# Kernel tuning notes

Measured on AMD Instinct MI355X. Metric: run time of the kernel, lower is better.

## Reference

```python
import jax, jax.numpy as jnp
import numpy as np

EMBED_DIM = 1024
B, T = 4, 2048

def setup_inputs() -> dict:
    key = jax.random.key(0)
    ks = jax.random.split(key, 7)
    s = 1.0 / np.sqrt(EMBED_DIM)
    return {
        "x": jax.random.normal(ks[0], (B, T, EMBED_DIM), dtype=jnp.float32),
        "Wq": jax.random.uniform(ks[1], (EMBED_DIM, EMBED_DIM), jnp.float32, -s, s),
        "bq": jax.random.uniform(ks[2], (EMBED_DIM,), jnp.float32, -s, s),
        "Wk": jax.random.uniform(ks[3], (EMBED_DIM, EMBED_DIM), jnp.float32, -s, s),
        "bk": jax.random.uniform(ks[4], (EMBED_DIM,), jnp.float32, -s, s),
        "Wv": jax.random.uniform(ks[5], (EMBED_DIM, EMBED_DIM), jnp.float32, -s, s),
        "bv": jax.random.uniform(ks[6], (EMBED_DIM,), jnp.float32, -s, s),
    }

def reference(x, Wq, bq, Wk, bk, Wv, bv):
    Bsz, Tlen, C = x.shape
    # torch Linear: y = x @ W.T + b
    Q = jnp.einsum('btc,dc->btd', x, Wq) + bq
    K = jnp.einsum('btc,dc->btd', x, Wk) + bk
    V = jnp.einsum('btc,dc->btd', x, Wv) + bv
    score = jnp.einsum('bqd,bkd->bqk', Q, K) / jnp.sqrt(jnp.float32(C))
    causal = jnp.tril(jnp.ones((Tlen, Tlen), dtype=bool))  # [T,T]
    score = jnp.where(causal, score, -jnp.inf)
    att = jax.nn.softmax(score, axis=-1)
    return jnp.einsum('bqk,bkd->bqd', att, V)
```

## Files before the change

kernel.cpp:

```cpp
#include <hip/hip_runtime.h>


using u16 = unsigned short;
typedef __attribute__((ext_vector_type(8))) short short8;
typedef __attribute__((ext_vector_type(4))) float f32x4;

__device__ __forceinline__ u16 f2b(float f) {
  unsigned u = __builtin_bit_cast(unsigned, f);
  u += 0x7fffu + ((u >> 16) & 1u);
  return (u16)(u >> 16);
}

__device__ __forceinline__ float b2f(u16 h) {
  return __builtin_bit_cast(float, (unsigned)h << 16);
}

__device__ __forceinline__ void async16(void* lds, const void* g) {
  __builtin_amdgcn_global_load_lds(
      (const __attribute__((address_space(1))) unsigned int*)g,
      (__attribute__((address_space(3))) unsigned int*)lds, 16, 0, 0);
}

__device__ __forceinline__ void block_barrier() {
  asm volatile("" ::: "memory");
  __builtin_amdgcn_s_barrier();
  asm volatile("" ::: "memory");
}

__global__ __launch_bounds__(256) void cvt_all_kernel(
    const float* __restrict__ x, const float* __restrict__ Wq,
    const float* __restrict__ Wk, const float* __restrict__ Wv,
    u16* __restrict__ xb, u16* __restrict__ Wcat) {
  const int i = blockIdx.x * 256 + threadIdx.x;
  const float* src;
  u16* dst;
  int c;
  if (i < 2097152) {
    src = x; dst = xb; c = i;
  } else {
    const int r = i - 2097152;
    const int seg = r >> 18;
    src = seg == 0 ? Wq : (seg == 1 ? Wk : Wv);
    dst = Wcat + (size_t)seg * 1048576;
    c = r & 262143;
  }
  const float4 v = reinterpret_cast<const float4*>(src)[c];
  ushort4 o;
  o.x = f2b(v.x); o.y = f2b(v.y); o.z = f2b(v.z); o.w = f2b(v.w);
  reinterpret_cast<ushort4*>(dst)[c] = o;
}

#define STG_A(buf, half, roff, ku)                                          \
  {                                                                         \
    async16(&Asm[buf][half][tid * 8], gA0 + (size_t)(roff)*lda + (ku));     \
    async16(&Asm[buf][half][4096 + tid * 8],                                \
            gA0 + (size_t)((roff) + 128) * lda + (ku));                     \
  }
#define STG_B(buf, half, roff, ku)                                          \
  {                                                                         \
    async16(&Bsm[buf][half][tid * 8], gB0 + (size_t)(roff)*ldb + (ku));     \
    async16(&Bsm[buf][half][4096 + tid * 8],                                \
            gB0 + (size_t)((roff) + 128) * ldb + (ku));                     \
  }
#define RD_A(buf, hh)                                                       \
  {                                                                         \
    _Pragma("unroll") for (int ii = 0; ii < 4; ++ii) {                      \
      a[ii][0] = *(const short8*)(&Asm[buf][hh][aoff + ii * 1024 + sk0]);   \
      a[ii][1] = *(const short8*)(&Asm[buf][hh][aoff + ii * 1024 + sk1]);   \
    }                                                                       \
  }
#define RD_B(buf, cc, breg)                                                 \
  {                                                                         \
    _Pragma("unroll") for (int jj = 0; jj < 2; ++jj) {                      \
      breg[jj][0] = *(const short8*)(&Bsm[buf][cc][boff + jj * 1024 + sk0]);\
      breg[jj][1] = *(const short8*)(&Bsm[buf][cc][boff + jj * 1024 + sk1]);\
    }                                                                       \
  }
#define QUAD(hh, cc, breg)                                                  \
  {                                                                         \
    __builtin_amdgcn_s_setprio(1);                                          \
    _Pragma("unroll") for (int ii = 0; ii < 4; ++ii)                        \
        _Pragma("unroll") for (int jj = 0; jj < 2; ++jj) {                  \
      acc[(hh)*4 + ii][(cc)*2 + jj] =                                       \
          __builtin_amdgcn_mfma_f32_16x16x32_bf16(                          \
              a[ii][0], breg[jj][0], acc[(hh)*4 + ii][(cc)*2 + jj], 0,0,0); \
      acc[(hh)*4 + ii][(cc)*2 + jj] =                                       \
          __builtin_amdgcn_mfma_f32_16x16x32_bf16(                          \
              a[ii][1], breg[jj][1], acc[(hh)*4 + ii][(cc)*2 + jj], 0,0,0); \
    }                                                                       \
    __builtin_amdgcn_s_setprio(0);                                          \
  }
#define LGK0 asm volatile("s_waitcnt lgkmcnt(0)" ::: "memory")
#define VM6 asm volatile("s_waitcnt vmcnt(6)" ::: "memory")

template <int NT, typename Epi>
__device__ __forceinline__ void gemm256_8ph(const u16* __restrict__ A, int lda,
                                            const u16* __restrict__ B, int ldb,
                                            Epi&& epi) {
  __shared__ __align__(16) u16 Asm[2][2][8192];
  __shared__ __align__(16) u16 Bsm[2][2][8192];
  const int tid = threadIdx.x;
  const int lane = tid & 63;
  const int w = tid >> 6;
  const int wm = w >> 2;
  const int wn = w & 3;

  f32x4 acc[8][4];
#pragma unroll
  for (int i = 0; i < 8; ++i)
#pragma unroll
    for (int j = 0; j < 4; ++j) acc[i][j] = f32x4{0.f, 0.f, 0.f, 0.f};

  const int sr = tid >> 3;
  const int ce = ((tid & 7) ^ (sr & 7)) << 3;
  const u16* gA0 = A + (size_t)sr * lda + ce;
  const int bE = (sr & 31) + ((sr >> 5) << 6);
  const u16* gB0 = B + (size_t)bE * ldb + ce;

  const int l15 = lane & 15;
  const int hi = lane >> 4;
  const int lo7 = lane & 7;
  const int aoff = wm * 4096 + l15 * 64;
  const int boff = wn * 2048 + l15 * 64;
  const int sk0 = (hi ^ lo7) << 3;
  const int sk1 = ((4 + hi) ^ lo7) << 3;

  short8 a[4][2], bEr[2][2], bLr[2][2];

  STG_A(0, 0, 0, 0); STG_B(0, 0, 0, 0); STG_A(0, 1, 64, 0); STG_B(0, 1, 32, 0);
  STG_A(1, 0, 0, 64); STG_B(1, 0, 0, 64); STG_A(1, 1, 64, 64);
  VM6;
  block_barrier();

  for (int t = 0; t < NT; t += 2) {
    const int k1 = (t + 1) * 64;
    const int t2c = (t + 2 < NT) ? (t + 2) : (NT - 1);
    const int t3c = (t + 3 < NT) ? (t + 3) : (NT - 1);
    const int k2 = t2c * 64;
    const int k3 = t3c * 64;
    RD_A(0, 0); RD_B(0, 0, bEr); STG_B(1, 1, 32, k1);
    block_barrier(); LGK0; QUAD(0, 0, bEr); block_barrier();
    RD_B(0, 1, bLr); STG_A(0, 0, 0, k2);
    block_barrier(); LGK0; QUAD(0, 1, bLr); block_barrier();
    RD_A(0, 1); STG_B(0, 0, 0, k2);
    block_barrier(); LGK0; QUAD(1, 1, bLr); block_barrier();
    STG_A(0, 1, 64, k2);
    VM6; block_barrier(); QUAD(1, 0, bEr); block_barrier();
    RD_A(1, 0); RD_B(1, 0, bEr); STG_B(0, 1, 32, k2);
    block_barrier(); LGK0; QUAD(0, 0, bEr); block_barrier();
    RD_B(1, 1, bLr); STG_A(1, 0, 0, k3);
    block_barrier(); LGK0; QUAD(0, 1, bLr); block_barrier();
    RD_A(1, 1); STG_B(1, 0, 0, k3);
    block_barrier(); LGK0; QUAD(1, 1, bLr); block_barrier();
    STG_A(1, 1, 64, k3);
    VM6; block_barrier(); QUAD(1, 0, bEr); block_barrier();
  }
  asm volatile("s_waitcnt vmcnt(0)" ::: "memory");
  epi(acc, wm, wn, lane);
}

__global__ __launch_bounds__(512, 1) void qkv_qk_kernel(
    const u16* __restrict__ xb, const u16* __restrict__ Wcat,
    const float* __restrict__ bq, const float* __restrict__ bk,
    u16* __restrict__ Qb, u16* __restrict__ Kb) {
  const int bid = blockIdx.x;
  const int swz = (bid & 7) * 32 + (bid >> 3);
  const int mt = swz >> 3, nt = swz & 7;
  const int z = nt >> 2;
  const float* bias = z ? bk : bq;
  u16* out = z ? Kb : Qb;
  const float scale = z ? 1.0f : 0.03125f;
  gemm256_8ph<16>(
      xb + (size_t)mt * 256 * 1024, 1024, Wcat + (size_t)nt * 256 * 1024, 1024,
      [&](f32x4(&acc)[8][4], int wm, int wn, int lane) {
        const int r0 = mt * 256 + wm * 128 + ((lane >> 4) << 2);
        const int c0 = (nt & 3) * 256 + wn * 64 + (lane & 15);
#pragma unroll
        for (int i8 = 0; i8 < 8; ++i8) {
          const int rb = r0 + (i8 >> 2) * 64 + (i8 & 3) * 16;
#pragma unroll
          for (int i4 = 0; i4 < 4; ++i4) {
            const int col = c0 + (i4 >> 1) * 32 + (i4 & 1) * 16;
            const float bb = bias[col];
#pragma unroll
            for (int rr = 0; rr < 4; ++rr)
              out[(size_t)(rb + rr) * 1024 + col] =
                  f2b((acc[i8][i4][rr] + bb) * scale);
          }
        }
      });
}

template <typename Epi>
__device__ __forceinline__ void gemm_bt_tile(const u16* __restrict__ A, int lda,
                                             const u16* __restrict__ B, int ldb,
                                             int nt, Epi&& epi) {
  __shared__ __align__(16) u16 As[128 * 64];
  __shared__ __align__(16) u16 Bs[128 * 64];
  const int tid = threadIdx.x;
  const int lane = tid & 63;
  const int w = tid >> 6;
  const int wr = (w >> 1) << 6;
  const int wc = (w & 1) << 6;

  f32x4 acc[4][4];
#pragma unroll
  for (int i = 0; i < 4; ++i)
#pragma unroll
    for (int j = 0; j < 4; ++j) acc[i][j] = f32x4{0.f, 0.f, 0.f, 0.f};

  const int sr = tid >> 3;
  const int ce = ((tid & 7) ^ (sr & 7)) << 3;
  const u16* gA = A + (size_t)sr * lda + ce;
  const u16* gB = B + (size_t)sr * ldb + ce;
  u16* const dA = As + tid * 8;
  u16* const dB = Bs + tid * 8;

  const int hi = lane >> 4;
  const int lo7 = lane & 7;
  const int ra = (wr + (lane & 15)) << 6;
  const int rb = (wc + (lane & 15)) << 6;
  const int sk0 = (hi ^ lo7) << 3;
  const int sk1 = ((4 + hi) ^ lo7) << 3;

  for (int t = 0; t < nt; ++t) {
    __syncthreads();
#pragma unroll
    for (int s = 0; s < 4; ++s) {
      async16(dA + s * 2048, gA + (size_t)(s * 32) * lda);
      async16(dB + s * 2048, gB + (size_t)(s * 32) * ldb);
    }
    gA += 64;
    gB += 64;
    __syncthreads();
#pragma unroll
    for (int kk = 0; kk < 2; ++kk) {
      const int sk = kk ? sk1 : sk0;
      short8 af[4], bf[4];
#pragma unroll
      for (int i = 0; i < 4; ++i)
        af[i] = *(const short8*)(As + ra + i * 1024 + sk);
#pragma unroll
      for (int j = 0; j < 4; ++j)
        bf[j] = *(const short8*)(Bs + rb + j * 1024 + sk);
#pragma unroll
      for (int i = 0; i < 4; ++i)
#pragma unroll
        for (int j = 0; j < 4; ++j)
          acc[i][j] = __builtin_amdgcn_mfma_f32_16x16x32_bf16(af[i], bf[j],
                                                              acc[i][j], 0, 0, 0);
    }
  }
  epi(acc, wr, wc, lane);
}

__global__ __launch_bounds__(256) void qkv_v_kernel(
    const u16* __restrict__ xb, const u16* __restrict__ Wcat,
    const float* __restrict__ bv, u16* __restrict__ Vtb) {
  const int bid = blockIdx.x;
  const int u = bid >> 3;
  const int nt = (bid & 7) * 8 + (u >> 3);
  const int mt = u & 7;
  const u16* Wvb = Wcat + (size_t)2 * 1048576;
  gemm_bt_tile(
      Wvb + (size_t)mt * 128 * 1024, 1024, xb + (size_t)nt * 128 * 1024, 1024, 16,
      [&](f32x4(&acc)[4][4], int wr, int wc, int lane) {
        const int r0 = mt * 128 + wr + ((lane >> 4) << 2);
        const int c0 = nt * 128 + wc + (lane & 15);
#pragma unroll
        for (int i = 0; i < 4; ++i)
#pragma unroll
          for (int rr = 0; rr < 4; ++rr) {
            const int row = r0 + i * 16 + rr;
            const float bb = bv[row];
#pragma unroll
            for (int j = 0; j < 4; ++j)
              Vtb[(size_t)row * 8192 + c0 + j * 16] = f2b(acc[i][j][rr] + bb);
          }
      });
}

__global__ __launch_bounds__(256) void score_kernel(const u16* __restrict__ Qb,
                                                    const u16* __restrict__ Kb,
                                                    u16* __restrict__ S) {
  const int b = blockIdx.y;
  const int t = blockIdx.x;
  int qt = 0;
  while ((qt + 1) * (qt + 2) / 2 <= t) ++qt;
  const int kt = t - (qt * (qt + 1)) / 2;
  const u16* A = Qb + ((size_t)b * 2048 + qt * 128) * 1024;
  const u16* Bp = Kb + ((size_t)b * 2048 + kt * 128) * 1024;
  u16* Sb = S + (size_t)b * 2048 * 2048;
  gemm_bt_tile(A, 1024, Bp, 1024, 16,
               [&](f32x4(&acc)[4][4], int wr, int wc, int lane) {
                 const int r0 = qt * 128 + wr + ((lane >> 4) << 2);
                 const int c0 = kt * 128 + wc + (lane & 15);
#pragma unroll
                 for (int i = 0; i < 4; ++i)
#pragma unroll
                   for (int j = 0; j < 4; ++j)
#pragma unroll
                     for (int rr = 0; rr < 4; ++rr)
                       Sb[(size_t)(r0 + i * 16 + rr) * 2048 + c0 + j * 16] =
                           f2b(acc[i][j][rr]);
               });
}

__global__ __launch_bounds__(256) void softmax_kernel(const u16* __restrict__ S,
                                                      u16* __restrict__ P) {
  __shared__ float redm[4], reds[4];
  const int rowid = blockIdx.x;
  const int b = rowid >> 11;
  const int q = rowid & 2047;
  const u16* Srow = S + ((size_t)b * 2048 + q) * 2048;
  u16* Prow = P + ((size_t)b * 2048 + q) * 2048;
  const int L = q + 1;
  const int Lpad = ((q >> 7) + 1) << 7;
  const int tid = threadIdx.x;
  const int k0 = tid << 3;
  const bool active = k0 < Lpad;
  float v[8];
  float m = -1e30f;
  if (active) {
    const short8 s8 = *(const short8*)(Srow + k0);
#pragma unroll
    for (int j = 0; j < 8; ++j) {
      v[j] = (k0 + j < L) ? b2f((u16)s8[j]) : -1e30f;
      m = fmaxf(m, v[j]);
    }
  }
#pragma unroll
  for (int o = 32; o > 0; o >>= 1) m = fmaxf(m, __shfl_xor(m, o));
  if ((tid & 63) == 0) redm[tid >> 6] = m;
  __syncthreads();
  m = fmaxf(fmaxf(redm[0], redm[1]), fmaxf(redm[2], redm[3]));
  float s = 0.f;
  if (active) {
#pragma unroll
    for (int j = 0; j < 8; ++j) {
      const float e = (k0 + j < L) ? __expf(v[j] - m) : 0.f;
      v[j] = e;
      s += e;
    }
  }
#pragma unroll
  for (int o = 32; o > 0; o >>= 1) s += __shfl_xor(s, o);
  if ((tid & 63) == 0) reds[tid >> 6] = s;
  __syncthreads();
  s = reds[0] + reds[1] + reds[2] + reds[3];
  const float inv = 1.0f / s;
  if (active) {
    short8 o8;
#pragma unroll
    for (int j = 0; j < 8; ++j)
      o8[j] = (short)((k0 + j < L) ? f2b(v[j] * inv) : (u16)0);
    *(short8*)(Prow + k0) = o8;
  }
}

__global__ __launch_bounds__(256) void pv_kernel(const u16* __restrict__ P,
                                                 const u16* __restrict__ Vtb,
                                                 float* __restrict__ O) {
  const int bid = blockIdx.x;
  const int pair = bid >> 8;
  const int idx = bid & 255;
  const int hb = idx >> 7;
  const int qt_raw = (idx >> 3) & 15;
  const int dt = idx & 7;
  const int qt = pair ? (15 - qt_raw) : qt_raw;
  const int b = pair * 2 + hb;
  const u16* A = P + (size_t)b * 2048 * 2048 + (size_t)qt * 128 * 2048;
  const u16* Bp = Vtb + (size_t)dt * 128 * 8192 + b * 2048;
  float* Ob = O + (size_t)b * 2048 * 1024;
  gemm_bt_tile(A, 2048, Bp, 8192, (qt + 1) * 2,
               [&](f32x4(&acc)[4][4], int wr, int wc, int lane) {
                 const int r0 = qt * 128 + wr + ((lane >> 4) << 2);
                 const int c0 = dt * 128 + wc + (lane & 15);
#pragma unroll
                 for (int i = 0; i < 4; ++i)
#pragma unroll
                   for (int j = 0; j < 4; ++j)
#pragma unroll
                     for (int rr = 0; rr < 4; ++rr)
                       Ob[(size_t)(r0 + i * 16 + rr) * 1024 + c0 + j * 16] =
                           acc[i][j][rr];
               });
}

extern "C" void kernel_launch(void* const* d_in, const int* in_sizes, int n_in,
                              void* d_out, int out_size, void* d_ws, size_t ws_size,
                              hipStream_t stream) {
  const float* x = (const float*)d_in[0];
  const float* Wq = (const float*)d_in[1];
  const float* bq = (const float*)d_in[2];
  const float* Wk = (const float*)d_in[3];
  const float* bk = (const float*)d_in[4];
  const float* Wv = (const float*)d_in[5];
  const float* bv = (const float*)d_in[6];
  float* out = (float*)d_out;
  char* ws = (char*)d_ws;
  u16* Qb = (u16*)(ws);
  u16* Kb = (u16*)(ws + (16u << 20));
  u16* Vtb = (u16*)(ws + (32u << 20));
  u16* xb = (u16*)(ws + (48u << 20));
  u16* Wcat = (u16*)(ws + (64u << 20));
  u16* S = (u16*)(ws + (70u << 20));
  u16* P = (u16*)(ws + (134u << 20));

  cvt_all_kernel<<<11264, 256, 0, stream>>>(x, Wq, Wk, Wv, xb, Wcat);
  qkv_qk_kernel<<<256, 512, 0, stream>>>(xb, Wcat, bq, bk, Qb, Kb);
  qkv_v_kernel<<<512, 256, 0, stream>>>(xb, Wcat, bv, Vtb);
  score_kernel<<<dim3(136, 4), 256, 0, stream>>>(Qb, Kb, S);
  softmax_kernel<<<8192, 256, 0, stream>>>(S, P);
  pv_kernel<<<512, 256, 0, stream>>>(P, Vtb, out);
}
```

Baseline: 162.4 us.

## Use 128-deep K tiles in PV GEMM and remap block scheduling orders

Adds a GEMM tile routine that stages 128 K-elements per iteration into two 64-wide LDS halves, halving the number of barrier pairs per tile, and uses it for the P·V kernel. The P·V block index is remapped to interleave long and short causal q-tiles across batches for load balance. The score kernel's triangular tile index is permuted with a stride to spread q-tiles across consecutive blocks. This doubles LDS use per block, which may reduce occupancy, and there is still no double buffering overlap.

```diff
diff --git a/kernel.cpp b/kernel.cpp
--- a/kernel.cpp
+++ b/kernel.cpp
@@ -254,6 +254,72 @@
   epi(acc, wr, wc, lane);
 }
 
+template <typename Epi>
+__device__ __forceinline__ void gemm_bt_128k(const u16* __restrict__ A, int lda,
+                                             const u16* __restrict__ B, int ldb,
+                                             int nt, Epi&& epi) {
+  __shared__ __align__(16) u16 As[2][128 * 64];
+  __shared__ __align__(16) u16 Bs[2][128 * 64];
+  const int tid = threadIdx.x;
+  const int lane = tid & 63;
+  const int w = tid >> 6;
+  const int wr = (w >> 1) << 6;
+  const int wc = (w & 1) << 6;
+
+  f32x4 acc[4][4];
+#pragma unroll
+  for (int i = 0; i < 4; ++i)
+#pragma unroll
+    for (int j = 0; j < 4; ++j) acc[i][j] = f32x4{0.f, 0.f, 0.f, 0.f};
+
+  const int sr = tid >> 3;
+  const int ce = ((tid & 7) ^ (sr & 7)) << 3;
+  const u16* gA = A + (size_t)sr * lda + ce;
+  const u16* gB = B + (size_t)sr * ldb + ce;
+
+  const int hi = lane >> 4;
+  const int lo7 = lane & 7;
+  const int ra = (wr + (lane & 15)) << 6;
+  const int rb = (wc + (lane & 15)) << 6;
+  const int sk0 = (hi ^ lo7) << 3;
+  const int sk1 = ((4 + hi) ^ lo7) << 3;
+
+  for (int t = 0; t < nt; ++t) {
+    __syncthreads();
+#pragma unroll
+    for (int kh = 0; kh < 2; ++kh)
+#pragma unroll
+      for (int s = 0; s < 4; ++s) {
+        async16(&As[kh][tid * 8 + s * 2048],
+                gA + kh * 64 + (size_t)(s * 32) * lda);
+        async16(&Bs[kh][tid * 8 + s * 2048],
+                gB + kh * 64 + (size_t)(s * 32) * ldb);
+      }
+    gA += 128;
+    gB += 128;
+    __syncthreads();
+#pragma unroll
+    for (int kk = 0; kk < 4; ++kk) {
+      const int kh = kk >> 1;
+      const int sk = (kk & 1) ? sk1 : sk0;
+      short8 af[4], bf[4];
+#pragma unroll
+      for (int i = 0; i < 4; ++i)
+        af[i] = *(const short8*)(&As[kh][ra + i * 1024 + sk]);
+#pragma unroll
+      for (int j = 0; j < 4; ++j)
+        bf[j] = *(const short8*)(&Bs[kh][rb + j * 1024 + sk]);
+#pragma unroll
+      for (int i = 0; i < 4; ++i)
+#pragma unroll
+        for (int j = 0; j < 4; ++j)
+          acc[i][j] = __builtin_amdgcn_mfma_f32_16x16x32_bf16(af[i], bf[j],
+                                                              acc[i][j], 0, 0, 0);
+    }
+  }
+  epi(acc, wr, wc, lane);
+}
+
 __global__ __launch_bounds__(256) void qkv_v_kernel(
     const u16* __restrict__ xb, const u16* __restrict__ Wcat,
     const float* __restrict__ bv, u16* __restrict__ Vtb) {
@@ -284,7 +350,8 @@
                                                     const u16* __restrict__ Kb,
                                                     u16* __restrict__ S) {
   const int b = blockIdx.y;
-  const int t = blockIdx.x;
+  const int traw = blockIdx.x;
+  const int t = (traw & 7) * 17 + (traw >> 3);
   int qt = 0;
   while ((qt + 1) * (qt + 2) / 2 <= t) ++qt;
   const int kt = t - (qt * (qt + 1)) / 2;
@@ -362,17 +429,15 @@
                                                  const u16* __restrict__ Vtb,
                                                  float* __restrict__ O) {
   const int bid = blockIdx.x;
-  const int pair = bid >> 8;
-  const int idx = bid & 255;
-  const int hb = idx >> 7;
-  const int qt_raw = (idx >> 3) & 15;
-  const int dt = idx & 7;
-  const int qt = pair ? (15 - qt_raw) : qt_raw;
-  const int b = pair * 2 + hb;
+  const int g = bid >> 5;
+  const int qt = (g & 1) ? ((g - 1) >> 1) : (15 - (g >> 1));
+  const int inner = bid & 31;
+  const int b = inner >> 3;
+  const int dt = inner & 7;
   const u16* A = P + (size_t)b * 2048 * 2048 + (size_t)qt * 128 * 2048;
   const u16* Bp = Vtb + (size_t)dt * 128 * 8192 + b * 2048;
   float* Ob = O + (size_t)b * 2048 * 1024;
-  gemm_bt_tile(A, 2048, Bp, 8192, (qt + 1) * 2,
+  gemm_bt_128k(A, 2048, Bp, 8192, qt + 1,
                [&](f32x4(&acc)[4][4], int wr, int wc, int lane) {
                  const int r0 = qt * 128 + wr + ((lane >> 4) << 2);
                  const int c0 = dt * 128 + wc + (lane & 15);
```

New measurement: 149.3 us. 8.1% less time.

## Double K-tile depth in bt GEMM, reorder score/PV block schedules, add lgkm wait

Applied to the files above, without the earlier changes.

The 128x128 bt GEMM now stages two 64-wide K slices (K=128) per iteration into doubled LDS buffers. This halves the number of sync/load rounds for the V-projection, score and PV kernels, at the cost of twice the LDS footprint. Score tiles are remapped with a stride permutation, and PV blocks interleave long and short query tiles across batches for better load balance and cache locality. In the 256 GEMM, a partial lgkmcnt wait is added after the first LDS reads of each half-iteration.

```diff
diff --git a/kernel.cpp b/kernel.cpp
--- a/kernel.cpp
+++ b/kernel.cpp
@@ -91,6 +91,7 @@
     __builtin_amdgcn_s_setprio(0);                                          \
   }
 #define LGK0 asm volatile("s_waitcnt lgkmcnt(0)" ::: "memory")
+#define LGK8 asm volatile("s_waitcnt lgkmcnt(8)" ::: "memory")
 #define VM6 asm volatile("s_waitcnt vmcnt(6)" ::: "memory")
 
 template <int NT, typename Epi>
@@ -138,7 +139,7 @@
     const int t3c = (t + 3 < NT) ? (t + 3) : (NT - 1);
     const int k2 = t2c * 64;
     const int k3 = t3c * 64;
-    RD_A(0, 0); RD_B(0, 0, bEr); STG_B(1, 1, 32, k1);
+    RD_A(0, 0); RD_B(0, 0, bEr); STG_B(1, 1, 32, k1); LGK8;
     block_barrier(); LGK0; QUAD(0, 0, bEr); block_barrier();
     RD_B(0, 1, bLr); STG_A(0, 0, 0, k2);
     block_barrier(); LGK0; QUAD(0, 1, bLr); block_barrier();
@@ -146,7 +147,7 @@
     block_barrier(); LGK0; QUAD(1, 1, bLr); block_barrier();
     STG_A(0, 1, 64, k2);
     VM6; block_barrier(); QUAD(1, 0, bEr); block_barrier();
-    RD_A(1, 0); RD_B(1, 0, bEr); STG_B(0, 1, 32, k2);
+    RD_A(1, 0); RD_B(1, 0, bEr); STG_B(0, 1, 32, k2); LGK8;
     block_barrier(); LGK0; QUAD(0, 0, bEr); block_barrier();
     RD_B(1, 1, bLr); STG_A(1, 0, 0, k3);
     block_barrier(); LGK0; QUAD(0, 1, bLr); block_barrier();
@@ -192,11 +193,11 @@
 }
 
 template <typename Epi>
-__device__ __forceinline__ void gemm_bt_tile(const u16* __restrict__ A, int lda,
+__device__ __forceinline__ void gemm_bt_128k(const u16* __restrict__ A, int lda,
                                              const u16* __restrict__ B, int ldb,
                                              int nt, Epi&& epi) {
-  __shared__ __align__(16) u16 As[128 * 64];
-  __shared__ __align__(16) u16 Bs[128 * 64];
+  __shared__ __align__(16) u16 As[2][128 * 64];
+  __shared__ __align__(16) u16 Bs[2][128 * 64];
   const int tid = threadIdx.x;
   const int lane = tid & 63;
   const int w = tid >> 6;
@@ -213,8 +214,6 @@
   const int ce = ((tid & 7) ^ (sr & 7)) << 3;
   const u16* gA = A + (size_t)sr * lda + ce;
   const u16* gB = B + (size_t)sr * ldb + ce;
-  u16* const dA = As + tid * 8;
-  u16* const dB = Bs + tid * 8;
 
   const int hi = lane >> 4;
   const int lo7 = lane & 7;
@@ -226,23 +225,28 @@
   for (int t = 0; t < nt; ++t) {
     __syncthreads();
 #pragma unroll
-    for (int s = 0; s < 4; ++s) {
-      async16(dA + s * 2048, gA + (size_t)(s * 32) * lda);
-      async16(dB + s * 2048, gB + (size_t)(s * 32) * ldb);
-    }
-    gA += 64;
-    gB += 64;
+    for (int kh = 0; kh < 2; ++kh)
+#pragma unroll
+      for (int s = 0; s < 4; ++s) {
+        async16(&As[kh][tid * 8 + s * 2048],
+                gA + kh * 64 + (size_t)(s * 32) * lda);
+        async16(&Bs[kh][tid * 8 + s * 2048],
+                gB + kh * 64 + (size_t)(s * 32) * ldb);
+      }
+    gA += 128;
+    gB += 128;
     __syncthreads();
 #pragma unroll
-    for (int kk = 0; kk < 2; ++kk) {
-      const int sk = kk ? sk1 : sk0;
+    for (int kk = 0; kk < 4; ++kk) {
+      const int kh = kk >> 1;
+      const int sk = (kk & 1) ? sk1 : sk0;
       short8 af[4], bf[4];
 #pragma unroll
       for (int i = 0; i < 4; ++i)
-        af[i] = *(const short8*)(As + ra + i * 1024 + sk);
+        af[i] = *(const short8*)(&As[kh][ra + i * 1024 + sk]);
 #pragma unroll
       for (int j = 0; j < 4; ++j)
-        bf[j] = *(const short8*)(Bs + rb + j * 1024 + sk);
+        bf[j] = *(const short8*)(&Bs[kh][rb + j * 1024 + sk]);
 #pragma unroll
       for (int i = 0; i < 4; ++i)
 #pragma unroll
@@ -262,8 +266,8 @@
   const int nt = (bid & 7) * 8 + (u >> 3);
   const int mt = u & 7;
   const u16* Wvb = Wcat + (size_t)2 * 1048576;
-  gemm_bt_tile(
-      Wvb + (size_t)mt * 128 * 1024, 1024, xb + (size_t)nt * 128 * 1024, 1024, 16,
+  gemm_bt_128k(
+      Wvb + (size_t)mt * 128 * 1024, 1024, xb + (size_t)nt * 128 * 1024, 1024, 8,
       [&](f32x4(&acc)[4][4], int wr, int wc, int lane) {
         const int r0 = mt * 128 + wr + ((lane >> 4) << 2);
         const int c0 = nt * 128 + wc + (lane & 15);
@@ -284,14 +288,15 @@
                                                     const u16* __restrict__ Kb,
                                                     u16* __restrict__ S) {
   const int b = blockIdx.y;
-  const int t = blockIdx.x;
+  const int traw = blockIdx.x;
+  const int t = (traw & 7) * 17 + (traw >> 3);
   int qt = 0;
   while ((qt + 1) * (qt + 2) / 2 <= t) ++qt;
   const int kt = t - (qt * (qt + 1)) / 2;
   const u16* A = Qb + ((size_t)b * 2048 + qt * 128) * 1024;
   const u16* Bp = Kb + ((size_t)b * 2048 + kt * 128) * 1024;
   u16* Sb = S + (size_t)b * 2048 * 2048;
-  gemm_bt_tile(A, 1024, Bp, 1024, 16,
+  gemm_bt_128k(A, 1024, Bp, 1024, 8,
                [&](f32x4(&acc)[4][4], int wr, int wc, int lane) {
                  const int r0 = qt * 128 + wr + ((lane >> 4) << 2);
                  const int c0 = kt * 128 + wc + (lane & 15);
@@ -362,17 +367,15 @@
                                                  const u16* __restrict__ Vtb,
                                                  float* __restrict__ O) {
   const int bid = blockIdx.x;
-  const int pair = bid >> 8;
-  const int idx = bid & 255;
-  const int hb = idx >> 7;
-  const int qt_raw = (idx >> 3) & 15;
-  const int dt = idx & 7;
-  const int qt = pair ? (15 - qt_raw) : qt_raw;
-  const int b = pair * 2 + hb;
+  const int g = bid >> 5;
+  const int qt = (g & 1) ? ((g - 1) >> 1) : (15 - (g >> 1));
+  const int inner = bid & 31;
+  const int b = inner >> 3;
+  const int dt = inner & 7;
   const u16* A = P + (size_t)b * 2048 * 2048 + (size_t)qt * 128 * 2048;
   const u16* Bp = Vtb + (size_t)dt * 128 * 8192 + b * 2048;
   float* Ob = O + (size_t)b * 2048 * 1024;
-  gemm_bt_tile(A, 2048, Bp, 8192, (qt + 1) * 2,
+  gemm_bt_128k(A, 2048, Bp, 8192, qt + 1,
                [&](f32x4(&acc)[4][4], int wr, int wc, int lane) {
                  const int r0 = qt * 128 + wr + ((lane >> 4) << 2);
                  const int c0 = dt * 128 + wc + (lane & 15);
```

After: 155.3 us. 4.4% less time.
